# Kernel tuning notes

Hardware: AMD Instinct MI355X
Metric: run time of the kernel (lower is better)

The kernel has to match this reference:

```python
import jax, jax.numpy as jnp
import numpy as np

BEAM_SIZE = 16


def setup_inputs() -> dict:
    key = jax.random.key(0)
    ks = jax.random.split(key, 9)
    B, N, S, A, Ai, E = 4, 48, 32, 16, 8, 512
    unaries = jax.random.normal(ks[0], (B, N, S), jnp.float32)
    behaviors = jax.random.normal(ks[1], (B, N, S, A), jnp.float32)
    interactions = jax.random.normal(ks[2], (B, N, N, S, S, Ai), jnp.float32)
    masks = jnp.ones((B, N), jnp.bool_)
    behavior_masks = jax.random.bernoulli(ks[3], 0.5, (S, A))
    interaction_masks = jax.random.bernoulli(ks[4], 0.5, (S, S, Ai))
    binary_edges = jax.random.randint(ks[5], (B, E, 2), 0, N, jnp.int32)
    binary_masks = jnp.ones((B, E), jnp.bool_)
    targets = jax.random.randint(ks[6], (B, N), 0, S, jnp.int32)
    weight_param_unary = jax.random.uniform(ks[7], (S,), jnp.float32)
    weight_param_binary = jax.random.uniform(ks[8], (S, S), jnp.float32)
    return dict(unaries=unaries, behaviors=behaviors, interactions=interactions,
                weight_param_unary=weight_param_unary, weight_param_binary=weight_param_binary,
                masks=masks, behavior_masks=behavior_masks, interaction_masks=interaction_masks,
                binary_edges=binary_edges, binary_masks=binary_masks, targets=targets)


def _forward(unaries, behaviors, interactions, weight_param_unary, weight_param_binary,
             masks, behavior_masks, interaction_masks, binary_edges, binary_masks, targets):
    sg = jax.lax.stop_gradient  # mirrors torch.no_grad blocks
    B, N, S = unaries.shape
    E = binary_edges.shape[1]
    K = min(BEAM_SIZE, S)
    dt = unaries.dtype

    m = masks[..., None].astype(dt)                                  # (B,N,1)
    masked_unaries = sg(unaries * m)                                 # no_grad
    bmask = behavior_masks.astype(dt)                                # (S,A)
    acnt = bmask.sum(-1)
    acnt = jnp.where(acnt == 0, jnp.ones((), dt), acnt)              # (S,)
    behaviors_unaries = sg(((behaviors * bmask).sum(-1) / acnt) * m) # (B,N,S), no_grad

    weighted_unaries = masked_unaries + weight_param_unary * behaviors_unaries

    # --- beam selection (targets forced to beam slot 0 via +inf scatter) ---
    bi = jnp.arange(B)[:, None]
    ni = jnp.arange(N)[None, :]
    _u = weighted_unaries.at[bi, ni, targets].set(jnp.inf)
    beam_targets = jax.lax.top_k(sg(_u), K)[1]                       # (B,N,K) int
    beam_unary = jnp.take_along_axis(weighted_unaries, beam_targets, axis=2)  # (B,N,K)

    # --- binary potentials: masked mean over interaction actions ---
    imask = interaction_masks.astype(dt)                             # (S,S,Ai)
    icnt = imask.sum(-1)
    icnt = jnp.where(icnt == 0, jnp.ones((), dt), icnt)              # (S,S)
    masked_inter = (interactions * imask).sum(-1) / icnt             # (B,N,N,S,S)

    eb = jnp.arange(B)[:, None]
    sel = masked_inter[eb, binary_edges[..., 0], binary_edges[..., 1]]  # (B,E,S,S)
    bt1 = beam_targets[eb, binary_edges[..., 0]]                     # (B,E,K)
    bt2 = beam_targets[eb, binary_edges[..., 1]]                     # (B,E,K)
    bin_phis_init = sg(sel[jnp.arange(B)[:, None, None, None],
                           jnp.arange(E)[None, :, None, None],
                           bt1[:, :, :, None], bt2[:, :, None, :]])  # (B,E,K,K), no_grad
    bin_phis = bin_phis_init * weight_param_binary[bt1[:, :, :, None], bt2[:, :, None, :]]

    # --- piecewise pseudo-likelihood loss ---
    norm_unary = jax.nn.log_softmax(beam_unary, axis=-1)
    gold_unary = jnp.where(masks, norm_unary[:, :, 0], jnp.zeros((), dt))
    pll = gold_unary.sum(-1)                                         # (B,)
    norm_bin = jax.nn.log_softmax(bin_phis.reshape(B, E, K * K), axis=-1).reshape(B, E, K, K)
    gold_bin = jnp.where(binary_masks, norm_bin[:, :, 0, 0], jnp.zeros((), dt))
    pll = pll + gold_bin.sum(-1)
    nll = -(pll / masks.sum(-1).astype(dt)).mean()
    return nll


def reference(unaries, behaviors, interactions, weight_param_unary, weight_param_binary,
              masks, behavior_masks, interaction_masks, binary_edges, binary_masks, targets):
    return _forward(unaries, behaviors, interactions, weight_param_unary, weight_param_binary,
                    masks, behavior_masks, interaction_masks, binary_edges, binary_masks, targets)
```

## Files before the change

### kernel.cpp

```cpp
#include <hip/hip_runtime.h>
#include <hip/hip_bf16.h>
#include <math.h>

#define BB 4
#define NN 48
#define SS 32
#define AA 16
#define AI 8
#define EE 512
#define KK 16
#define NNODE (BB * NN)
#define NEDGE (BB * EE)

#define WS_CBIN  0
#define WS_BEAM  32768
#define WS_NG    45056
#define WS_EG    46080

__device__ __forceinline__ bool read_mask(const void* p, int idx, int flag) {
    if (flag == 1) return ((const unsigned char*)p)[idx] != 0;
    if (flag == 2) return ((const float*)p)[idx] != 0.0f;
    return ((const int*)p)[idx] != 0;
}

__device__ __forceinline__ int detect_flag(const void* bmask, int lane) {
    unsigned int wrd = ((const unsigned int*)bmask)[lane & 31];
    bool anyF = __any(wrd == 0x3F800000u);
    bool anyG = __any(wrd > 1u);
    return anyF ? 2 : (anyG ? 1 : 0);
}

__global__ __launch_bounds__(256) void node_kernel(
    const float* __restrict__ unaries,
    const float* __restrict__ behaviors,
    const float* __restrict__ wpu,
    const float* __restrict__ wpb,
    const void* masks, const void* bmask, const void* imask,
    const int* __restrict__ targets,
    float* __restrict__ cbin,
    int* __restrict__ beam,
    float* __restrict__ node_gold)
{
    int tid = threadIdx.x;
    int wid = tid >> 6, lane = tid & 63;
    int flag = detect_flag(bmask, lane);

    if (blockIdx.x < 48) {
        int node = blockIdx.x * 4 + wid;
        float m = read_mask(masks, node, flag) ? 1.f : 0.f;
        int tgt = targets[node];

        float val = -INFINITY, key = -INFINITY;
        if (lane < SS) {
            int s = lane;
            float u = unaries[node * SS + s];

            const float4* bp4 = (const float4*)(behaviors + ((size_t)node * SS + s) * AA);
            float4 b0 = bp4[0], b1 = bp4[1], b2 = bp4[2], b3 = bp4[3];
            float bv[16] = {b0.x,b0.y,b0.z,b0.w, b1.x,b1.y,b1.z,b1.w,
                            b2.x,b2.y,b2.z,b2.w, b3.x,b3.y,b3.z,b3.w};

            float bmv[16];
            if (flag == 1) {
                uint4 v = *(const uint4*)((const unsigned char*)bmask + s * 16);
                unsigned int w4[4] = {v.x, v.y, v.z, v.w};
                #pragma unroll
                for (int k = 0; k < 16; ++k)
                    bmv[k] = ((w4[k >> 2] >> ((k & 3) * 8)) & 255u) ? 1.f : 0.f;
            } else if (flag == 0) {
                const uint4* ip = (const uint4*)((const int*)bmask + s * 16);
                #pragma unroll
                for (int r = 0; r < 4; ++r) {
                    uint4 v = ip[r];
                    bmv[r*4+0] = v.x ? 1.f : 0.f; bmv[r*4+1] = v.y ? 1.f : 0.f;
                    bmv[r*4+2] = v.z ? 1.f : 0.f; bmv[r*4+3] = v.w ? 1.f : 0.f;
                }
            } else {
                const float4* fp = (const float4*)((const float*)bmask + s * 16);
                #pragma unroll
                for (int r = 0; r < 4; ++r) {
                    float4 v = fp[r];
                    bmv[r*4+0] = v.x != 0.f ? 1.f : 0.f; bmv[r*4+1] = v.y != 0.f ? 1.f : 0.f;
                    bmv[r*4+2] = v.z != 0.f ? 1.f : 0.f; bmv[r*4+3] = v.w != 0.f ? 1.f : 0.f;
                }
            }

            float cnt = 0.f, raw = 0.f;
            #pragma unroll
            for (int k = 0; k < 16; ++k) { cnt += bmv[k]; raw += bmv[k] * bv[k]; }
            if (cnt == 0.f) cnt = 1.f;
            val = m * (u + wpu[s] * (raw / cnt));
            key = (s == tgt) ? INFINITY : val;
        }

        int rank = 0;
        #pragma unroll
        for (int t = 0; t < SS; ++t) {
            float kt = __shfl(key, t, 64);
            rank += (kt > key) || (kt == key && t < lane);
        }
        bool sel = (lane < SS) && (rank < KK);

        bool sel_nt = sel && (lane != tgt);
        unsigned long long bal = __ballot(sel_nt);
        if (sel) {
            int slot = (lane == tgt) ? 0
                       : 1 + __popcll(bal & ((1ull << lane) - 1ull));
            beam[node * KK + slot] = lane;
        }

        float mv = sel ? val : -INFINITY;
        #pragma unroll
        for (int off = 32; off >= 1; off >>= 1)
            mv = fmaxf(mv, __shfl_xor(mv, off, 64));
        float se = sel ? expf(val - mv) : 0.f;
        #pragma unroll
        for (int off = 32; off >= 1; off >>= 1)
            se += __shfl_xor(se, off, 64);
        float vt = __shfl(val, tgt, 64);
        if (lane == 0)
            node_gold[node] = (m > 0.f) ? (vt - mv - logf(se)) : 0.f;
    } else {
        int p = (blockIdx.x - 48) * 256 + tid;
        float imv[8];
        if (flag == 1) {
            uint2 v = *(const uint2*)((const unsigned char*)imask + p * 8);
            unsigned int w2[2] = {v.x, v.y};
            #pragma unroll
            for (int k = 0; k < 8; ++k)
                imv[k] = ((w2[k >> 2] >> ((k & 3) * 8)) & 255u) ? 1.f : 0.f;
        } else if (flag == 0) {
            const uint4* ip = (const uint4*)((const int*)imask + p * 8);
            uint4 v0 = ip[0], v1 = ip[1];
            imv[0]=v0.x?1.f:0.f; imv[1]=v0.y?1.f:0.f; imv[2]=v0.z?1.f:0.f; imv[3]=v0.w?1.f:0.f;
            imv[4]=v1.x?1.f:0.f; imv[5]=v1.y?1.f:0.f; imv[6]=v1.z?1.f:0.f; imv[7]=v1.w?1.f:0.f;
        } else {
            const float4* fp = (const float4*)((const float*)imask + p * 8);
            float4 v0 = fp[0], v1 = fp[1];
            imv[0]=v0.x!=0.f?1.f:0.f; imv[1]=v0.y!=0.f?1.f:0.f; imv[2]=v0.z!=0.f?1.f:0.f; imv[3]=v0.w!=0.f?1.f:0.f;
            imv[4]=v1.x!=0.f?1.f:0.f; imv[5]=v1.y!=0.f?1.f:0.f; imv[6]=v1.z!=0.f?1.f:0.f; imv[7]=v1.w!=0.f?1.f:0.f;
        }
        float cnt = imv[0]+imv[1]+imv[2]+imv[3]+imv[4]+imv[5]+imv[6]+imv[7];
        if (cnt == 0.f) cnt = 1.f;
        float w = wpb[p] / cnt;
        float4 o0 = make_float4(imv[0]*w, imv[1]*w, imv[2]*w, imv[3]*w);
        float4 o1 = make_float4(imv[4]*w, imv[5]*w, imv[6]*w, imv[7]*w);
        *(float4*)(cbin + p * AI)     = o0;
        *(float4*)(cbin + p * AI + 4) = o1;
    }
}

__global__ __launch_bounds__(512) void edge_kernel(
    const float* __restrict__ interactions,
    const int* __restrict__ edges,
    const void* binmask, const void* bmask,
    const float* __restrict__ cbin,
    const int* __restrict__ beam,
    float* __restrict__ edge_gold)
{
    int tid = threadIdx.x;
    int le = tid >> 8;
    int t  = tid & 255;
    int wid = tid >> 6;
    int lane = tid & 63;
    int be = (blockIdx.x << 1) + le;
    int b = be >> 9;

    int2 e2 = ((const int2*)edges)[be];
    int n1 = e2.x, n2 = e2.y;

    int i = t >> 4, j = t & 15;
    int s1 = beam[(b * NN + n1) * KK + i];
    int s2 = beam[(b * NN + n2) * KK + j];
    int p = s1 * SS + s2;

    size_t base = (((size_t)(b * NN + n1) * NN + n2) * (SS * SS) + p) * AI;
    float4 x0 = *(const float4*)(interactions + base);
    float4 x1 = *(const float4*)(interactions + base + 4);
    float4 c0 = *(const float4*)(cbin + p * AI);
    float4 c1 = *(const float4*)(cbin + p * AI + 4);
    float phi = x0.x * c0.x + x0.y * c0.y + x0.z * c0.z + x0.w * c0.w
              + x1.x * c1.x + x1.y * c1.y + x1.z * c1.z + x1.w * c1.w;

    float mw = phi;
    #pragma unroll
    for (int off = 32; off >= 1; off >>= 1)
        mw = fmaxf(mw, __shfl_xor(mw, off, 64));
    float ew = expf(phi - mw);
    #pragma unroll
    for (int off = 32; off >= 1; off >>= 1)
        ew += __shfl_xor(ew, off, 64);

    __shared__ float2 sred[8];
    if (lane == 0) sred[wid] = make_float2(mw, ew);
    __syncthreads();

    if (t == 0) {
        int w0 = le << 2;
        float2 p0 = sred[w0], p1 = sred[w0+1], p2 = sred[w0+2], p3 = sred[w0+3];
        float M = fmaxf(fmaxf(p0.x, p1.x), fmaxf(p2.x, p3.x));
        float S = p0.y * expf(p0.x - M) + p1.y * expf(p1.x - M)
                + p2.y * expf(p2.x - M) + p3.y * expf(p3.x - M);
        float gold = phi - M - logf(S);
        int flag = detect_flag(bmask, lane);
        bool bm = read_mask(binmask, be, flag);
        edge_gold[be] = bm ? gold : 0.f;
    }
}

__global__ __launch_bounds__(256) void final_kernel(
    const void* masks, const void* bmask,
    const float* __restrict__ node_gold,
    const float* __restrict__ edge_gold,
    float* __restrict__ out)
{
    int tid = threadIdx.x;
    int b = tid >> 6;
    int lane = tid & 63;
    int flag = detect_flag(bmask, lane);

    float sum = 0.f, cnt = 0.f;
    if (lane < NN) {
        sum += node_gold[b * NN + lane];
        cnt += read_mask(masks, b * NN + lane, flag) ? 1.f : 0.f;
    }
    for (int e = lane; e < EE; e += 64)
        sum += edge_gold[b * EE + e];

    #pragma unroll
    for (int off = 32; off >= 1; off >>= 1) {
        sum += __shfl_xor(sum, off, 64);
        cnt += __shfl_xor(cnt, off, 64);
    }
    __shared__ float sp[4];
    if (lane == 0) sp[b] = sum / cnt;
    __syncthreads();
    if (tid == 0)
        out[0] = -(sp[0] + sp[1] + sp[2] + sp[3]) * (1.f / BB);
}

extern "C" void kernel_launch(void* const* d_in, const int* in_sizes, int n_in,
                              void* d_out, int out_size, void* d_ws, size_t ws_size,
                              hipStream_t stream) {
    const float* unaries      = (const float*)d_in[0];
    const float* behaviors    = (const float*)d_in[1];
    const float* interactions = (const float*)d_in[2];
    const float* wpu          = (const float*)d_in[3];
    const float* wpb          = (const float*)d_in[4];
    const void*  masks        = d_in[5];
    const void*  bmask        = d_in[6];
    const void*  imask        = d_in[7];
    const int*   edges        = (const int*)d_in[8];
    const void*  binmask      = d_in[9];
    const int*   targets      = (const int*)d_in[10];
    float* out = (float*)d_out;

    char* ws = (char*)d_ws;
    float* cbin      = (float*)(ws + WS_CBIN);
    int*   beamp     = (int*)(ws + WS_BEAM);
    float* node_gold = (float*)(ws + WS_NG);
    float* edge_gold = (float*)(ws + WS_EG);

    node_kernel<<<52, 256, 0, stream>>>(unaries, behaviors, wpu, wpb,
                                        masks, bmask, imask, targets,
                                        cbin, beamp, node_gold);
    edge_kernel<<<NEDGE / 2, 512, 0, stream>>>(interactions, edges, binmask,
                                               bmask, cbin, beamp, edge_gold);
    final_kernel<<<1, 256, 0, stream>>>(masks, bmask, node_gold, edge_gold, out);
}
```

Measured before the change: 20.25 us.

## Fuse node beam selection into edge kernel, recomputing beams per edge block

Merges the node and edge kernels into one launch. Each edge block recomputes the beams of its two endpoint nodes in shared memory, and a third wavefront writes node gold values for the first 192 blocks. It also computes the interaction-mask weighting inline instead of reading a precomputed cbin buffer. This removes one kernel launch and the global round trip for beam and cbin, at the cost of redundant beam computation and extra behaviors and mask reads per edge.

After: 17.59 us. 1.15x faster.

```diff
diff --git a/kernel.cpp b/kernel.cpp
--- a/kernel.cpp
+++ b/kernel.cpp
@@ -12,10 +12,8 @@
 #define NNODE (BB * NN)
 #define NEDGE (BB * EE)
 
-#define WS_CBIN  0
-#define WS_BEAM  32768
-#define WS_NG    45056
-#define WS_EG    46080
+#define WS_NG    0
+#define WS_EG    1024
 
 __device__ __forceinline__ bool read_mask(const void* p, int idx, int flag) {
     if (flag == 1) return ((const unsigned char*)p)[idx] != 0;
@@ -30,85 +28,78 @@
     return anyF ? 2 : (anyG ? 1 : 0);
 }
 
-__global__ __launch_bounds__(256) void node_kernel(
-    const float* __restrict__ unaries,
-    const float* __restrict__ behaviors,
-    const float* __restrict__ wpu,
-    const float* __restrict__ wpb,
-    const void* masks, const void* bmask, const void* imask,
-    const int* __restrict__ targets,
-    float* __restrict__ cbin,
-    int* __restrict__ beam,
-    float* __restrict__ node_gold)
+__device__ __forceinline__ void node_beam(
+    int node, int lane, int flag,
+    const float* __restrict__ unaries, const float* __restrict__ behaviors,
+    const void* masks, const int* __restrict__ targets,
+    const float* __restrict__ wpu, const void* bmask,
+    int* beam16, float* gold_out)
 {
-    int tid = threadIdx.x;
-    int wid = tid >> 6, lane = tid & 63;
-    int flag = detect_flag(bmask, lane);
-
-    if (blockIdx.x < 48) {
-        int node = blockIdx.x * 4 + wid;
-        float m = read_mask(masks, node, flag) ? 1.f : 0.f;
-        int tgt = targets[node];
-
-        float val = -INFINITY, key = -INFINITY;
-        if (lane < SS) {
-            int s = lane;
-            float u = unaries[node * SS + s];
-
-            const float4* bp4 = (const float4*)(behaviors + ((size_t)node * SS + s) * AA);
-            float4 b0 = bp4[0], b1 = bp4[1], b2 = bp4[2], b3 = bp4[3];
-            float bv[16] = {b0.x,b0.y,b0.z,b0.w, b1.x,b1.y,b1.z,b1.w,
-                            b2.x,b2.y,b2.z,b2.w, b3.x,b3.y,b3.z,b3.w};
-
-            float bmv[16];
-            if (flag == 1) {
-                uint4 v = *(const uint4*)((const unsigned char*)bmask + s * 16);
-                unsigned int w4[4] = {v.x, v.y, v.z, v.w};
-                #pragma unroll
-                for (int k = 0; k < 16; ++k)
-                    bmv[k] = ((w4[k >> 2] >> ((k & 3) * 8)) & 255u) ? 1.f : 0.f;
-            } else if (flag == 0) {
-                const uint4* ip = (const uint4*)((const int*)bmask + s * 16);
-                #pragma unroll
-                for (int r = 0; r < 4; ++r) {
-                    uint4 v = ip[r];
-                    bmv[r*4+0] = v.x ? 1.f : 0.f; bmv[r*4+1] = v.y ? 1.f : 0.f;
-                    bmv[r*4+2] = v.z ? 1.f : 0.f; bmv[r*4+3] = v.w ? 1.f : 0.f;
-                }
-            } else {
-                const float4* fp = (const float4*)((const float*)bmask + s * 16);
-                #pragma unroll
-                for (int r = 0; r < 4; ++r) {
-                    float4 v = fp[r];
-                    bmv[r*4+0] = v.x != 0.f ? 1.f : 0.f; bmv[r*4+1] = v.y != 0.f ? 1.f : 0.f;
-                    bmv[r*4+2] = v.z != 0.f ? 1.f : 0.f; bmv[r*4+3] = v.w != 0.f ? 1.f : 0.f;
-                }
+    float m = read_mask(masks, node, flag) ? 1.f : 0.f;
+    int tgt = targets[node];
+
+    float val = -INFINITY, key = -INFINITY;
+    if (lane < SS) {
+        int s = lane;
+        float u = unaries[node * SS + s];
+
+        const float4* bp4 = (const float4*)(behaviors + ((size_t)node * SS + s) * AA);
+        float4 b0 = bp4[0], b1 = bp4[1], b2 = bp4[2], b3 = bp4[3];
+        float bv[16] = {b0.x,b0.y,b0.z,b0.w, b1.x,b1.y,b1.z,b1.w,
+                        b2.x,b2.y,b2.z,b2.w, b3.x,b3.y,b3.z,b3.w};
+
+        float bmv[16];
+        if (flag == 1) {
+            uint4 v = *(const uint4*)((const unsigned char*)bmask + s * 16);
+            unsigned int w4[4] = {v.x, v.y, v.z, v.w};
+            #pragma unroll
+            for (int k = 0; k < 16; ++k)
+                bmv[k] = ((w4[k >> 2] >> ((k & 3) * 8)) & 255u) ? 1.f : 0.f;
+        } else if (flag == 0) {
+            const uint4* ip = (const uint4*)((const int*)bmask + s * 16);
+            #pragma unroll
+            for (int r = 0; r < 4; ++r) {
+                uint4 v = ip[r];
+                bmv[r*4+0] = v.x ? 1.f : 0.f; bmv[r*4+1] = v.y ? 1.f : 0.f;
+                bmv[r*4+2] = v.z ? 1.f : 0.f; bmv[r*4+3] = v.w ? 1.f : 0.f;
             }
-
-            float cnt = 0.f, raw = 0.f;
+        } else {
+            const float4* fp = (const float4*)((const float*)bmask + s * 16);
             #pragma unroll
-            for (int k = 0; k < 16; ++k) { cnt += bmv[k]; raw += bmv[k] * bv[k]; }
-            if (cnt == 0.f) cnt = 1.f;
-            val = m * (u + wpu[s] * (raw / cnt));
-            key = (s == tgt) ? INFINITY : val;
+            for (int r = 0; r < 4; ++r) {
+                float4 v = fp[r];
+                bmv[r*4+0] = v.x != 0.f ? 1.f : 0.f; bmv[r*4+1] = v.y != 0.f ? 1.f : 0.f;
+                bmv[r*4+2] = v.z != 0.f ? 1.f : 0.f; bmv[r*4+3] = v.w != 0.f ? 1.f : 0.f;
+            }
         }
 
-        int rank = 0;
-        #pragma unroll
-        for (int t = 0; t < SS; ++t) {
-            float kt = __shfl(key, t, 64);
-            rank += (kt > key) || (kt == key && t < lane);
-        }
-        bool sel = (lane < SS) && (rank < KK);
-
+        float cnt = 0.f, raw = 0.f;
+        #pragma unroll
+        for (int k = 0; k < 16; ++k) { cnt += bmv[k]; raw += bmv[k] * bv[k]; }
+        if (cnt == 0.f) cnt = 1.f;
+        val = m * (u + wpu[s] * (raw / cnt));
+        key = (s == tgt) ? INFINITY : val;
+    }
+
+    int rank = 0;
+    #pragma unroll
+    for (int t = 0; t < SS; ++t) {
+        float kt = __shfl(key, t, 64);
+        rank += (kt > key) || (kt == key && t < lane);
+    }
+    bool sel = (lane < SS) && (rank < KK);
+
+    if (beam16) {
         bool sel_nt = sel && (lane != tgt);
         unsigned long long bal = __ballot(sel_nt);
         if (sel) {
             int slot = (lane == tgt) ? 0
                        : 1 + __popcll(bal & ((1ull << lane) - 1ull));
-            beam[node * KK + slot] = lane;
+            beam16[slot] = lane;
         }
-
+    }
+
+    if (gold_out) {
         float mv = sel ? val : -INFINITY;
         #pragma unroll
         for (int off = 32; off >= 1; off >>= 1)
@@ -119,68 +110,76 @@
             se += __shfl_xor(se, off, 64);
         float vt = __shfl(val, tgt, 64);
         if (lane == 0)
-            node_gold[node] = (m > 0.f) ? (vt - mv - logf(se)) : 0.f;
-    } else {
-        int p = (blockIdx.x - 48) * 256 + tid;
-        float imv[8];
-        if (flag == 1) {
-            uint2 v = *(const uint2*)((const unsigned char*)imask + p * 8);
-            unsigned int w2[2] = {v.x, v.y};
-            #pragma unroll
-            for (int k = 0; k < 8; ++k)
-                imv[k] = ((w2[k >> 2] >> ((k & 3) * 8)) & 255u) ? 1.f : 0.f;
-        } else if (flag == 0) {
-            const uint4* ip = (const uint4*)((const int*)imask + p * 8);
-            uint4 v0 = ip[0], v1 = ip[1];
-            imv[0]=v0.x?1.f:0.f; imv[1]=v0.y?1.f:0.f; imv[2]=v0.z?1.f:0.f; imv[3]=v0.w?1.f:0.f;
-            imv[4]=v1.x?1.f:0.f; imv[5]=v1.y?1.f:0.f; imv[6]=v1.z?1.f:0.f; imv[7]=v1.w?1.f:0.f;
-        } else {
-            const float4* fp = (const float4*)((const float*)imask + p * 8);
-            float4 v0 = fp[0], v1 = fp[1];
-            imv[0]=v0.x!=0.f?1.f:0.f; imv[1]=v0.y!=0.f?1.f:0.f; imv[2]=v0.z!=0.f?1.f:0.f; imv[3]=v0.w!=0.f?1.f:0.f;
-            imv[4]=v1.x!=0.f?1.f:0.f; imv[5]=v1.y!=0.f?1.f:0.f; imv[6]=v1.z!=0.f?1.f:0.f; imv[7]=v1.w!=0.f?1.f:0.f;
-        }
-        float cnt = imv[0]+imv[1]+imv[2]+imv[3]+imv[4]+imv[5]+imv[6]+imv[7];
-        if (cnt == 0.f) cnt = 1.f;
-        float w = wpb[p] / cnt;
-        float4 o0 = make_float4(imv[0]*w, imv[1]*w, imv[2]*w, imv[3]*w);
-        float4 o1 = make_float4(imv[4]*w, imv[5]*w, imv[6]*w, imv[7]*w);
-        *(float4*)(cbin + p * AI)     = o0;
-        *(float4*)(cbin + p * AI + 4) = o1;
-    }
-}
-
-__global__ __launch_bounds__(512) void edge_kernel(
+            *gold_out = (m > 0.f) ? (vt - mv - logf(se)) : 0.f;
+    }
+}
+
+__global__ __launch_bounds__(256) void main_kernel(
+    const float* __restrict__ unaries,
+    const float* __restrict__ behaviors,
     const float* __restrict__ interactions,
-    const int* __restrict__ edges,
-    const void* binmask, const void* bmask,
-    const float* __restrict__ cbin,
-    const int* __restrict__ beam,
+    const float* __restrict__ wpu,
+    const float* __restrict__ wpb,
+    const void* masks, const void* bmask, const void* imask,
+    const int* __restrict__ edges, const void* binmask,
+    const int* __restrict__ targets,
+    float* __restrict__ node_gold,
     float* __restrict__ edge_gold)
 {
+    int be = blockIdx.x;
+    int b = be >> 9;
     int tid = threadIdx.x;
-    int le = tid >> 8;
-    int t  = tid & 255;
-    int wid = tid >> 6;
-    int lane = tid & 63;
-    int be = (blockIdx.x << 1) + le;
-    int b = be >> 9;
+    int wid = tid >> 6, lane = tid & 63;
+    int flag = detect_flag(bmask, lane);
 
     int2 e2 = ((const int2*)edges)[be];
     int n1 = e2.x, n2 = e2.y;
 
-    int i = t >> 4, j = t & 15;
-    int s1 = beam[(b * NN + n1) * KK + i];
-    int s2 = beam[(b * NN + n2) * KK + j];
+    __shared__ int beamA[KK], beamB[KK];
+
+    bool active = (wid < 2) || (wid == 2 && be < NNODE);
+    if (active) {
+        int node = (wid == 0) ? (b * NN + n1)
+                 : (wid == 1) ? (b * NN + n2) : be;
+        int* bptr = (wid == 0) ? beamA : (wid == 1) ? beamB : nullptr;
+        float* gptr = (wid == 2) ? &node_gold[be] : nullptr;
+        node_beam(node, lane, flag, unaries, behaviors, masks, targets,
+                  wpu, bmask, bptr, gptr);
+    }
+    __syncthreads();
+
+    int i = tid >> 4, j = tid & 15;
+    int s1 = beamA[i], s2 = beamB[j];
     int p = s1 * SS + s2;
 
     size_t base = (((size_t)(b * NN + n1) * NN + n2) * (SS * SS) + p) * AI;
     float4 x0 = *(const float4*)(interactions + base);
     float4 x1 = *(const float4*)(interactions + base + 4);
-    float4 c0 = *(const float4*)(cbin + p * AI);
-    float4 c1 = *(const float4*)(cbin + p * AI + 4);
-    float phi = x0.x * c0.x + x0.y * c0.y + x0.z * c0.z + x0.w * c0.w
-              + x1.x * c1.x + x1.y * c1.y + x1.z * c1.z + x1.w * c1.w;
+    float xv[8] = {x0.x,x0.y,x0.z,x0.w, x1.x,x1.y,x1.z,x1.w};
+
+    float imv[8];
+    if (flag == 1) {
+        uint2 v = *(const uint2*)((const unsigned char*)imask + p * 8);
+        unsigned int w2[2] = {v.x, v.y};
+        #pragma unroll
+        for (int k = 0; k < 8; ++k)
+            imv[k] = ((w2[k >> 2] >> ((k & 3) * 8)) & 255u) ? 1.f : 0.f;
+    } else if (flag == 0) {
+        const uint4* ip = (const uint4*)((const int*)imask + p * 8);
+        uint4 v0 = ip[0], v1 = ip[1];
+        imv[0]=v0.x?1.f:0.f; imv[1]=v0.y?1.f:0.f; imv[2]=v0.z?1.f:0.f; imv[3]=v0.w?1.f:0.f;
+        imv[4]=v1.x?1.f:0.f; imv[5]=v1.y?1.f:0.f; imv[6]=v1.z?1.f:0.f; imv[7]=v1.w?1.f:0.f;
+    } else {
+        const float4* fp = (const float4*)((const float*)imask + p * 8);
+        float4 v0 = fp[0], v1 = fp[1];
+        imv[0]=v0.x!=0.f?1.f:0.f; imv[1]=v0.y!=0.f?1.f:0.f; imv[2]=v0.z!=0.f?1.f:0.f; imv[3]=v0.w!=0.f?1.f:0.f;
+        imv[4]=v1.x!=0.f?1.f:0.f; imv[5]=v1.y!=0.f?1.f:0.f; imv[6]=v1.z!=0.f?1.f:0.f; imv[7]=v1.w!=0.f?1.f:0.f;
+    }
+    float cnt = 0.f, raw = 0.f;
+    #pragma unroll
+    for (int k = 0; k < 8; ++k) { cnt += imv[k]; raw += imv[k] * xv[k]; }
+    if (cnt == 0.f) cnt = 1.f;
+    float phi = wpb[p] * (raw / cnt);
 
     float mw = phi;
     #pragma unroll
@@ -191,18 +190,16 @@
     for (int off = 32; off >= 1; off >>= 1)
         ew += __shfl_xor(ew, off, 64);
 
-    __shared__ float2 sred[8];
+    __shared__ float2 sred[4];
     if (lane == 0) sred[wid] = make_float2(mw, ew);
     __syncthreads();
 
-    if (t == 0) {
-        int w0 = le << 2;
-        float2 p0 = sred[w0], p1 = sred[w0+1], p2 = sred[w0+2], p3 = sred[w0+3];
+    if (tid == 0) {
+        float2 p0 = sred[0], p1 = sred[1], p2 = sred[2], p3 = sred[3];
         float M = fmaxf(fmaxf(p0.x, p1.x), fmaxf(p2.x, p3.x));
         float S = p0.y * expf(p0.x - M) + p1.y * expf(p1.x - M)
                 + p2.y * expf(p2.x - M) + p3.y * expf(p3.x - M);
         float gold = phi - M - logf(S);
-        int flag = detect_flag(bmask, lane);
         bool bm = read_mask(binmask, be, flag);
         edge_gold[be] = bm ? gold : 0.f;
     }
@@ -256,15 +253,12 @@
     float* out = (float*)d_out;
 
     char* ws = (char*)d_ws;
-    float* cbin      = (float*)(ws + WS_CBIN);
-    int*   beamp     = (int*)(ws + WS_BEAM);
     float* node_gold = (float*)(ws + WS_NG);
     float* edge_gold = (float*)(ws + WS_EG);
 
-    node_kernel<<<52, 256, 0, stream>>>(unaries, behaviors, wpu, wpb,
-                                        masks, bmask, imask, targets,
-                                        cbin, beamp, node_gold);
-    edge_kernel<<<NEDGE / 2, 512, 0, stream>>>(interactions, edges, binmask,
-                                               bmask, cbin, beamp, edge_gold);
+    main_kernel<<<NEDGE, 256, 0, stream>>>(unaries, behaviors, interactions,
+                                           wpu, wpb, masks, bmask, imask,
+                                           edges, binmask, targets,
+                                           node_gold, edge_gold);
     final_kernel<<<1, 256, 0, stream>>>(masks, bmask, node_gold, edge_gold, out);
 }
```
